# Kernel optimization log

Hardware: AMD Instinct MI355X
Metric: run time of the kernel (lower is better)

## Reference

```python
import jax, jax.numpy as jnp
import numpy as np

NPOINT = 2048  # S after transition-down (init npoint)
NSAMPLE = 16   # K neighbors (init nsample)
EPS = 1e-5     # BatchNorm eps


def _conv1d(w, b, x):  # w [O,I], x [B,I,N] -> [B,O,N]
    y = jnp.einsum('oi,bin->bon', w, x)
    return y if b is None else y + b[None, :, None]


def _conv2d(w, b, x):  # w [O,I], x [B,I,S,K] -> [B,O,S,K]
    y = jnp.einsum('oi,bisk->bosk', w, x)
    return y if b is None else y + b[None, :, None, None]


def _gather(x, idx):  # x [B,C,N], idx [B,S] -> [B,C,S]
    return jax.vmap(lambda xb, ib: xb[:, ib])(x, idx)


def _group(x, idx):  # x [B,C,N], idx [B,S,K] -> [B,C,S,K]
    return jax.vmap(lambda xb, ib: xb[:, ib])(x, idx)


def _fps(xyz_bnc, S):  # farthest point sampling, start at index 0 (deterministic)
    B, N, _ = xyz_bnc.shape
    def body(carry, _):
        dist, far = carry
        centroid = jnp.take_along_axis(xyz_bnc, far[:, None, None], axis=1)  # [B,1,3]
        d = jnp.sum((xyz_bnc - centroid) ** 2, axis=-1)  # [B,N]
        dist = jnp.minimum(dist, d)
        nxt = jnp.argmax(dist, axis=-1).astype(jnp.int32)
        return (dist, nxt), far
    init = (jnp.full((B, N), 1e10, xyz_bnc.dtype), jnp.zeros((B,), jnp.int32))
    _, idxs = jax.lax.scan(body, init, None, length=S)
    return jnp.transpose(idxs)  # [B,S]


def _knn(k, query, pts):  # query [B,S,3], pts [B,N,3] -> idx [B,S,k]
    d2 = (jnp.sum(query ** 2, -1)[..., None] + jnp.sum(pts ** 2, -1)[:, None, :]
          - 2.0 * jnp.einsum('bsc,bnc->bsn', query, pts))
    _, idx = jax.lax.top_k(-d2, k)
    return idx


def _bn(x, gamma, beta):  # training-mode batchnorm over (B, spatial) per channel
    axes = (0,) + tuple(range(2, x.ndim))
    m = jnp.mean(x, axes, keepdims=True)
    v = jnp.var(x, axes, keepdims=True)
    shp = (1, -1) + (1,) * (x.ndim - 2)
    return gamma.reshape(shp) * (x - m) / jnp.sqrt(v + EPS) + beta.reshape(shp)


def _forward(xyz, points, td_w, td_b, td_gamma, td_beta,
             blk_before_w, blk_before_b, blk_qkv_w,
             blk_pos_w1, blk_pos_b1, blk_pos_w2, blk_pos_b2,
             blk_attn_w1, blk_attn_b1, blk_attn_w2, blk_attn_b2,
             blk_after_w, blk_after_b):
    S, K = NPOINT, NSAMPLE
    xyz_t = jnp.transpose(xyz, (0, 2, 1))  # [B,N,3]
    # ---- PointTransformerTransitionDown ----
    fps_idx = _fps(xyz_t, S)                       # [B,S]
    new_xyz = _gather(xyz, fps_idx)                # [B,3,S]
    new_xyz_t = jnp.transpose(new_xyz, (0, 2, 1))  # [B,S,3]
    gidx = _knn(K, new_xyz_t, xyz_t)               # [B,S,K]
    grouped_xyz = _group(xyz, gidx) - new_xyz[:, :, :, None]   # [B,3,S,K]
    grouped = jnp.concatenate([_group(points, gidx), grouped_xyz], axis=1)  # [B,D+3,S,K]
    h = jax.nn.relu(_bn(_conv2d(td_w, td_b, grouped), td_gamma, td_beta))
    pts = jnp.max(h, axis=-1)  # [B,out,S]
    # ---- PointTransformerResBlocks ----
    sgidx = _knn(K, new_xyz_t, new_xyz_t)          # self-KNN [B,S,K]
    gxyz = new_xyz[:, :, :, None] - _group(new_xyz, sgidx)  # [B,3,S,K]
    num_attn = blk_before_w.shape[0]
    for i in range(num_attn):
        rel = _conv2d(blk_pos_w2[i], blk_pos_b2[i],
                      jax.nn.relu(_conv2d(blk_pos_w1[i], blk_pos_b1[i], gxyz)))  # [B,mid,S,K]
        p = _conv1d(blk_before_w[i], blk_before_b[i], pts)   # [B,mid,S]
        qkv = _conv1d(blk_qkv_w[i], None, p)                 # [B,3*mid,S]
        q, k_, v = jnp.split(qkv, 3, axis=1)
        qk_rel = q[:, :, :, None] - _group(k_, sgidx)        # [B,mid,S,K]
        v = _group(v, sgidx) + rel
        sim = _conv2d(blk_attn_w2[i], blk_attn_b2[i],
                      jax.nn.relu(_conv2d(blk_attn_w1[i], blk_attn_b1[i], qk_rel + rel)))
        attn = jax.nn.softmax(sim, axis=-1)                  # softmax over neighbors
        agg = jnp.sum(attn * v, axis=-1)                     # [B,mid,S]
        pts = pts + _conv1d(blk_after_w[i], blk_after_b[i], agg)
    return new_xyz, pts


def setup_inputs() -> dict:
    key = jax.random.key(0)
    ks = jax.random.split(key, 20)
    B, N, Din, Dout, mid, A = 4, 8192, 64, 128, 32, 2
    r = lambda k, s, sc: sc * jax.random.normal(k, s, dtype=jnp.float32)
    return {
        'xyz': r(ks[0], (B, 3, N), 1.0),
        'points': r(ks[1], (B, Din, N), 1.0),
        'td_w': r(ks[2], (Dout, Din + 3), 0.1), 'td_b': r(ks[3], (Dout,), 0.02),
        'td_gamma': jnp.ones((Dout,), jnp.float32), 'td_beta': jnp.zeros((Dout,), jnp.float32),
        'blk_before_w': r(ks[4], (A, mid, Dout), 0.1), 'blk_before_b': r(ks[5], (A, mid), 0.02),
        'blk_qkv_w': r(ks[6], (A, 3 * mid, mid), 0.1),
        'blk_pos_w1': r(ks[7], (A, 64, 3), 0.1), 'blk_pos_b1': r(ks[8], (A, 64), 0.02),
        'blk_pos_w2': r(ks[9], (A, mid, 64), 0.1), 'blk_pos_b2': r(ks[10], (A, mid), 0.02),
        'blk_attn_w1': r(ks[11], (A, 4 * mid, mid), 0.1), 'blk_attn_b1': r(ks[12], (A, 4 * mid), 0.02),
        'blk_attn_w2': r(ks[13], (A, mid, 4 * mid), 0.1), 'blk_attn_b2': r(ks[14], (A, mid), 0.02),
        'blk_after_w': r(ks[15], (A, Dout, mid), 0.1), 'blk_after_b': r(ks[16], (A, Dout), 0.02),
    }


def reference(xyz, points, td_w, td_b, td_gamma, td_beta,
              blk_before_w, blk_before_b, blk_qkv_w,
              blk_pos_w1, blk_pos_b1, blk_pos_w2, blk_pos_b2,
              blk_attn_w1, blk_attn_b1, blk_attn_w2, blk_attn_b2,
              blk_after_w, blk_after_b):
    return _forward(xyz, points, td_w, td_b, td_gamma, td_beta,
                    blk_before_w, blk_before_b, blk_qkv_w,
                    blk_pos_w1, blk_pos_b1, blk_pos_w2, blk_pos_b2,
                    blk_attn_w1, blk_attn_b1, blk_attn_w2, blk_attn_b2,
                    blk_after_w, blk_after_b)
```

## Files before the change

### kernel.cpp

```cpp
#include <hip/hip_runtime.h>

#define BB 4
#define NN 8192
#define SS 2048
#define KK 16

typedef float v2f __attribute__((ext_vector_type(2)));

#define FTH 512
#define FPT (NN/FTH)
__global__ __launch_bounds__(FTH, 1) void fps_kernel(
    const float* __restrict__ xyz,
    float* __restrict__ out_newxyz,
    float* __restrict__ nxt)
{
  #pragma clang fp contract(off)
  const int b = blockIdx.x;
  const int tid = threadIdx.x;
  const int wave = tid >> 6;
  const int lane = tid & 63;
  const float* xb = xyz + b*3*NN;
  __shared__ float sx[NN], sy[NN], sz[NN];
  __shared__ __align__(16) unsigned long long skey[2][8];
  __shared__ int smi[SS];
  v2f px[FPT/2], py[FPT/2], pz[FPT/2], dist[FPT/2];
  #pragma unroll
  for (int j = 0; j < FPT; ++j) {
    int i = tid + j*FTH;
    float x = xb[i], y = xb[NN+i], z = xb[2*NN+i];
    asm volatile("" : "+v"(x), "+v"(y), "+v"(z));
    ((float*)px)[j] = x; ((float*)py)[j] = y; ((float*)pz)[j] = z;
    ((float*)dist)[j] = 1e10f;
  }
  #pragma unroll
  for (int j = 0; j < FPT; ++j) {
    int i = tid + j*FTH;
    sx[i] = ((float*)px)[j]; sy[i] = ((float*)py)[j]; sz[i] = ((float*)pz)[j];
  }
  if (tid == 0) smi[0] = 0;
  int ic[FPT];
  #pragma unroll
  for (int j = 0; j < FPT; ++j) ic[j] = tid + j*FTH;
  float cx = xb[0], cy = xb[NN], cz = xb[2*NN];
  __syncthreads();
  for (int it = 1; it < SS; ++it) {
    const int buf = it & 1;
    v2f cx2 = {cx, cx}, cy2 = {cy, cy}, cz2 = {cz, cz};
    v2f vmax = {-1.0f, -1.0f};
    #pragma unroll
    for (int j = 0; j < FPT/2; ++j) {
      v2f dx = px[j] - cx2, dy = py[j] - cy2, dz = pz[j] - cz2;
      v2f d = dx*dx + dy*dy;
      d = d + dz*dz;
      v2f nd = __builtin_elementwise_min(dist[j], d);
      dist[j] = nd;
      vmax = __builtin_elementwise_max(vmax, nd);
    }
    float mloc = fmaxf(vmax.x, vmax.y);
    int besti = 0x7FFFFFFF;
    #pragma unroll
    for (int j = FPT/2 - 1; j >= 0; --j) {
      if (dist[j].y == mloc) besti = ic[2*j+1];
      if (dist[j].x == mloc) besti = ic[2*j];
    }
    unsigned khi = __float_as_uint(mloc);
    unsigned klo = ~(unsigned)besti;
    #define FPS_RED(ctrl) { \
      unsigned nlo = (unsigned)__builtin_amdgcn_update_dpp(0, (int)klo, ctrl, 0xf, 0xf, true); \
      unsigned nhi = (unsigned)__builtin_amdgcn_update_dpp(0, (int)khi, ctrl, 0xf, 0xf, true); \
      unsigned long long nk = ((unsigned long long)nhi << 32) | nlo; \
      unsigned long long ck = ((unsigned long long)khi << 32) | klo; \
      if (nk > ck) { khi = nhi; klo = nlo; } }
    FPS_RED(0x111)
    FPS_RED(0x112)
    FPS_RED(0x114)
    FPS_RED(0x118)
    FPS_RED(0x142)
    FPS_RED(0x143)
    #undef FPS_RED
    if (lane == 63) skey[buf][wave] = ((unsigned long long)khi << 32) | klo;
    __syncthreads();
    const ulonglong2* kp = (const ulonglong2*)&skey[buf][0];
    ulonglong2 k01 = kp[0], k23 = kp[1], k45 = kp[2], k67 = kp[3];
    unsigned long long m0 = k01.x > k01.y ? k01.x : k01.y;
    unsigned long long m1 = k23.x > k23.y ? k23.x : k23.y;
    unsigned long long m2 = k45.x > k45.y ? k45.x : k45.y;
    unsigned long long m3 = k67.x > k67.y ? k67.x : k67.y;
    unsigned long long ma = m0 > m1 ? m0 : m1;
    unsigned long long mb = m2 > m3 ? m2 : m3;
    unsigned long long mk = ma > mb ? ma : mb;
    int mi = (int)(~(unsigned)mk);
    if (tid == 0) smi[it] = mi;
    cx = sx[mi]; cy = sy[mi]; cz = sz[mi];
  }
  __syncthreads();
  for (int it = tid; it < SS; it += FTH) {
    int mi = smi[it];
    float x = sx[mi], y = sy[mi], z = sz[mi];
    out_newxyz[(b*3+0)*SS + it] = x;
    out_newxyz[(b*3+1)*SS + it] = y;
    out_newxyz[(b*3+2)*SS + it] = z;
    nxt[(b*SS+it)*3+0] = x; nxt[(b*SS+it)*3+1] = y; nxt[(b*SS+it)*3+2] = z;
  }
}

__global__ __launch_bounds__(256) void transpose_pts(
    const float* __restrict__ p, float* __restrict__ o)
{
  __shared__ float tile[32][33];
  const int b = blockIdx.z;
  const int n0 = blockIdx.x*32, c0 = blockIdx.y*32;
  const int x = threadIdx.x, y = threadIdx.y;
  #pragma unroll
  for (int i = y; i < 32; i += 8)
    tile[i][x] = p[(b*64 + c0+i)*NN + n0+x];
  __syncthreads();
  #pragma unroll
  for (int i = y; i < 32; i += 8)
    o[(b*NN + n0+i)*64 + c0+x] = tile[x][i];
}

#define TILE 2048
#define KTH 512
__global__ __launch_bounds__(KTH) void knn_kernel(
    const float* __restrict__ query_t,
    const float* __restrict__ cand1,
    const float* __restrict__ cand2,
    int* __restrict__ out1,
    int* __restrict__ out2)
{
  #pragma clang fp contract(off)
  __shared__ float4 sc[TILE];
  __shared__ float  smd[8*64*17];
  __shared__ int    smj[8*64*17];
  const int blocksPerB = SS/64;
  const int half = blockIdx.x >> 7;
  const int blk = blockIdx.x & 127;
  const float* cand = half ? cand2 : cand1;
  const int Nc = half ? SS : NN;
  int* outidx = half ? out2 : out1;
  const int b = blk / blocksPerB;
  const int q0 = (blk % blocksPerB)*64;
  const int wave = threadIdx.x >> 6, lane = threadIdx.x & 63;
  const int s = q0 + lane;
  const float qx = query_t[(b*SS+s)*3+0];
  const float qy = query_t[(b*SS+s)*3+1];
  const float qz = query_t[(b*SS+s)*3+2];
  float sq = qx*qx + qy*qy; sq = sq + qz*qz;
  float d16[16]; int i16[16];
  #pragma unroll
  for (int j = 0; j < 16; ++j) { d16[j] = 1e30f; i16[j] = 0x7FFFFFFF; }
  const float* cb = cand + b*3*Nc;
  const int QL = TILE/8;
  for (int base = 0; base < Nc; base += TILE) {
    __syncthreads();
    for (int j = threadIdx.x; j < TILE; j += KTH) {
      float x = cb[base+j], y = cb[Nc+base+j], z = cb[2*Nc+base+j];
      float pp = x*x + y*y; pp = pp + z*z;
      sc[j] = make_float4(x, y, z, pp);
    }
    __syncthreads();
    const int lo = wave*QL, hi = lo + QL;
    for (int j = lo; j < hi; ++j) {
      float4 c = sc[j];
      float qp = qx*c.x + qy*c.y; qp = qp + qz*c.z;
      float d2 = (sq + c.w) - 2.0f*qp;
      if (d2 < d16[15]) {
        d16[15] = d2; i16[15] = base + j;
        #pragma unroll
        for (int t = 15; t > 0; --t) {
          if (d16[t] < d16[t-1]) {
            float td = d16[t]; d16[t] = d16[t-1]; d16[t-1] = td;
            int   ti = i16[t]; i16[t] = i16[t-1]; i16[t-1] = ti;
          }
        }
      }
    }
  }
  const int off = (wave*64 + lane)*17;
  #pragma unroll
  for (int j = 0; j < 16; ++j) { smd[off+j] = d16[j]; smj[off+j] = i16[j]; }
  __syncthreads();
  if (wave == 0) {
    int p[8] = {0,0,0,0,0,0,0,0};
    for (int o = 0; o < 16; ++o) {
      float bd = 3e38f; int bi = 0x7FFFFFFF, bw = 0;
      #pragma unroll
      for (int w = 0; w < 8; ++w) {
        float d = smd[(w*64+lane)*17 + p[w]];
        int   i = smj[(w*64+lane)*17 + p[w]];
        if (d < bd || (d == bd && i < bi)) { bd = d; bi = i; bw = w; }
      }
      p[bw]++;
      outidx[(b*SS+s)*KK + o] = bi;
    }
  }
}

__global__ __launch_bounds__(128) void td_kernel(
    const float* __restrict__ ptst,
    const float* __restrict__ xyz,
    const float* __restrict__ newxyz,
    const int* __restrict__ gidx,
    const float* __restrict__ td_w,
    const float* __restrict__ td_b,
    float* __restrict__ ymax,
    float* __restrict__ psum,
    float* __restrict__ psq)
{
  const int bs = blockIdx.x;
  const int b = bs >> 11, s = bs & (SS-1);
  const int t = threadIdx.x;
  __shared__ int gi[KK];
  __shared__ float g[67*17];
  if (t < KK) gi[t] = gidx[bs*KK + t];
  __syncthreads();
  #pragma unroll
  for (int base = 0; base < 1024; base += 128) {
    int idx = base + t;
    int i = idx & 63, k = idx >> 6;
    g[i*17 + k] = ptst[(b*NN + gi[k])*64 + i];
  }
  if (t < 48) {
    int c = t >> 4, k = t & 15;
    g[(64+c)*17 + k] = xyz[(b*3+c)*NN + gi[k]] - newxyz[(b*3+c)*SS + s];
  }
  __syncthreads();
  float acc[KK];
  #pragma unroll
  for (int k = 0; k < KK; ++k) acc[k] = 0.0f;
  const float* wrow = td_w + t*67;
  for (int i = 0; i < 67; ++i) {
    float w = wrow[i];
    #pragma unroll
    for (int k = 0; k < KK; ++k) acc[k] = fmaf(w, g[i*17 + k], acc[k]);
  }
  float bias = td_b[t];
  float mx = -1e30f, s1 = 0.f, s2 = 0.f;
  #pragma unroll
  for (int k = 0; k < KK; ++k) {
    float y = acc[k] + bias;
    mx = fmaxf(mx, y);
    s1 += y;
    s2 = fmaf(y, y, s2);
  }
  ymax[bs*128 + t] = mx;
  psum[bs*128 + t] = s1;
  psq [bs*128 + t] = s2;
}

__global__ __launch_bounds__(256) void bn_partial(
    const float* __restrict__ psum, const float* __restrict__ psq,
    float* __restrict__ part1, float* __restrict__ part2)
{
  const int blk = blockIdx.x, t = threadIdx.x;
  const int c = t & 127, half = t >> 7;
  const float* ps = psum + (blk*64 + half*32)*128;
  const float* pq = psq  + (blk*64 + half*32)*128;
  float s1 = 0.f, s2 = 0.f;
  for (int r = 0; r < 32; ++r) { s1 += ps[r*128 + c]; s2 += pq[r*128 + c]; }
  __shared__ float sh1[256], sh2[256];
  sh1[t] = s1; sh2[t] = s2;
  __syncthreads();
  if (t < 128) {
    part1[blk*128 + t] = sh1[t] + sh1[t+128];
    part2[blk*128 + t] = sh2[t] + sh2[t+128];
  }
}

__global__ __launch_bounds__(128) void bn_final(
    const float* __restrict__ part1, const float* __restrict__ part2,
    const float* __restrict__ gamma, const float* __restrict__ beta,
    float* __restrict__ scale, float* __restrict__ bias)
{
  const int o = threadIdx.x;
  float s1 = 0.f, s2 = 0.f;
  for (int j = 0; j < 128; ++j) { s1 += part1[j*128+o]; s2 += part2[j*128+o]; }
  const float n = (float)(BB*SS*KK);
  float mean = s1/n;
  float var  = s2/n - mean*mean;
  float sc = gamma[o] / sqrtf(var + 1e-5f);
  scale[o] = sc;
  bias[o]  = beta[o] - mean*sc;
}

__global__ __launch_bounds__(128) void r1_first(
    const float* __restrict__ ymax,
    const float* __restrict__ scale, const float* __restrict__ bias,
    const float* __restrict__ bw, const float* __restrict__ bb,
    const float* __restrict__ qw,
    float* __restrict__ pts,
    float* __restrict__ qkv)
{
  const int bs = blockIdx.x;
  const int t = threadIdx.x;
  __shared__ float pcol[128];
  __shared__ float p[32];
  float v = fmaxf(fmaf(ymax[bs*128 + t], scale[t], bias[t]), 0.0f);
  pts[bs*128 + t] = v;
  pcol[t] = v;
  __syncthreads();
  if (t < 32) {
    float acc = 0.f;
    const float* w = bw + t*128;
    for (int j = 0; j < 128; ++j) acc = fmaf(w[j], pcol[j], acc);
    p[t] = acc + bb[t];
  }
  __syncthreads();
  if (t < 96) {
    float acc = 0.f;
    const float* w = qw + t*32;
    #pragma unroll
    for (int j = 0; j < 32; ++j) acc = fmaf(w[j], p[j], acc);
    qkv[bs*96 + t] = acc;
  }
}

__global__ __launch_bounds__(128) void r1_kernel(
    const float* __restrict__ pts,
    const float* __restrict__ bw, const float* __restrict__ bb,
    const float* __restrict__ qw,
    float* __restrict__ qkv)
{
  const int bs = blockIdx.x;
  const int t = threadIdx.x;
  __shared__ float pcol[128];
  __shared__ float p[32];
  pcol[t] = pts[bs*128 + t];
  __syncthreads();
  if (t < 32) {
    float acc = 0.f;
    const float* w = bw + t*128;
    for (int j = 0; j < 128; ++j) acc = fmaf(w[j], pcol[j], acc);
    p[t] = acc + bb[t];
  }
  __syncthreads();
  if (t < 96) {
    float acc = 0.f;
    const float* w = qw + t*32;
    #pragma unroll
    for (int j = 0; j < 32; ++j) acc = fmaf(w[j], p[j], acc);
    qkv[bs*96 + t] = acc;
  }
}

__global__ __launch_bounds__(128) void r2_kernel(
    const float* __restrict__ qkv,
    const float* __restrict__ newxyz,
    const int* __restrict__ sgidx,
    const float* __restrict__ pw1, const float* __restrict__ pb1,
    const float* __restrict__ pw2, const float* __restrict__ pb2,
    const float* __restrict__ aw1, const float* __restrict__ ab1,
    const float* __restrict__ aw2, const float* __restrict__ ab2,
    const float* __restrict__ fw,  const float* __restrict__ fb,
    float* __restrict__ pts)
{
  const int bs = blockIdx.x;
  const int b = bs >> 11, s = bs & (SS-1);
  const int t = threadIdx.x;
  __shared__ int sgi[KK];
  __shared__ float qv[32];
  __shared__ float kn[32*17], vn[32*17];
  __shared__ float gx[3*KK];
  __shared__ float h1[64*KK];
  __shared__ float x2[32*KK];
  __shared__ float a1[128*17];
  __shared__ float simb[32*KK];
  __shared__ float agg[32];
  if (t < KK) sgi[t] = sgidx[bs*KK + t];
  __syncthreads();
  if (t < 32) qv[t] = qkv[bs*96 + t];
  for (int idx = t; idx < 32*KK; idx += 128) {
    int k = idx >> 5, c = idx & 31;
    int base = (b*SS + sgi[k])*96;
    kn[c*17+k] = qkv[base + 32 + c];
    vn[c*17+k] = qkv[base + 64 + c];
  }
  if (t < 3*KK) {
    int c = t >> 4, k = t & 15;
    gx[t] = newxyz[(b*3+c)*SS + s] - newxyz[(b*3+c)*SS + sgi[k]];
  }
  __syncthreads();
  for (int idx = t; idx < 64*KK; idx += 128) {
    int c = idx >> 4, k = idx & 15;
    float acc = 0.f;
    #pragma unroll
    for (int j = 0; j < 3; ++j) acc = fmaf(pw1[c*3+j], gx[j*KK+k], acc);
    h1[idx] = fmaxf(acc + pb1[c], 0.0f);
  }
  __syncthreads();
  for (int idx = t; idx < 32*KK; idx += 128) {
    int c = idx >> 4, k = idx & 15;
    float acc = 0.f;
    const float* w = pw2 + c*64;
    for (int j = 0; j < 64; ++j) acc = fmaf(w[j], h1[j*KK+k], acc);
    float r = acc + pb2[c];
    x2[idx] = (qv[c] - kn[c*17+k]) + r;
    vn[c*17+k] = vn[c*17+k] + r;
  }
  __syncthreads();
  {
    float acc[KK];
    #pragma unroll
    for (int k = 0; k < KK; ++k) acc[k] = 0.f;
    const float* w = aw1 + t*32;
    for (int j = 0; j < 32; ++j) {
      float wv = w[j];
      #pragma unroll
      for (int k = 0; k < KK; ++k) acc[k] = fmaf(wv, x2[j*KK+k], acc[k]);
    }
    float bv = ab1[t];
    #pragma unroll
    for (int k = 0; k < KK; ++k) a1[t*17+k] = fmaxf(acc[k] + bv, 0.0f);
  }
  __syncthreads();
  for (int idx = t; idx < 32*KK; idx += 128) {
    int c = idx >> 4, k = idx & 15;
    float acc = 0.f;
    const float* w = aw2 + c*128;
    for (int j = 0; j < 128; ++j) acc = fmaf(w[j], a1[j*17+k], acc);
    simb[idx] = acc + ab2[c];
  }
  __syncthreads();
  if (t < 32) {
    float m = -1e30f;
    #pragma unroll
    for (int k = 0; k < KK; ++k) m = fmaxf(m, simb[t*KK+k]);
    float sum = 0.f;
    float e[KK];
    #pragma unroll
    for (int k = 0; k < KK; ++k) { e[k] = __expf(simb[t*KK+k] - m); sum += e[k]; }
    float inv = 1.0f / sum;
    float a = 0.f;
    #pragma unroll
    for (int k = 0; k < KK; ++k) a = fmaf(e[k]*inv, vn[t*17+k], a);
    agg[t] = a;
  }
  __syncthreads();
  {
    float acc = 0.f;
    const float* w = fw + t*32;
    #pragma unroll
    for (int j = 0; j < 32; ++j) acc = fmaf(w[j], agg[j], acc);
    pts[bs*128 + t] += acc + fb[t];
  }
}

__global__ __launch_bounds__(256) void transpose_out(
    const float* __restrict__ pts, float* __restrict__ out)
{
  __shared__ float tile[32][33];
  const int b = blockIdx.z;
  const int s0 = blockIdx.x*32, c0 = blockIdx.y*32;
  const int x = threadIdx.x, y = threadIdx.y;
  #pragma unroll
  for (int i = y; i < 32; i += 8)
    tile[i][x] = pts[(b*SS + s0+i)*128 + c0+x];
  __syncthreads();
  #pragma unroll
  for (int i = y; i < 32; i += 8)
    out[(b*128 + c0+i)*SS + s0 + x] = tile[x][i];
}

extern "C" void kernel_launch(void* const* d_in, const int* in_sizes, int n_in,
                              void* d_out, int out_size, void* d_ws, size_t ws_size,
                              hipStream_t stream) {
  const float* xyz      = (const float*)d_in[0];
  const float* points   = (const float*)d_in[1];
  const float* td_w     = (const float*)d_in[2];
  const float* td_b     = (const float*)d_in[3];
  const float* td_gamma = (const float*)d_in[4];
  const float* td_beta  = (const float*)d_in[5];
  const float* bw  = (const float*)d_in[6];
  const float* bb  = (const float*)d_in[7];
  const float* qw  = (const float*)d_in[8];
  const float* pw1 = (const float*)d_in[9];
  const float* pb1 = (const float*)d_in[10];
  const float* pw2 = (const float*)d_in[11];
  const float* pb2 = (const float*)d_in[12];
  const float* aw1 = (const float*)d_in[13];
  const float* ab1 = (const float*)d_in[14];
  const float* aw2 = (const float*)d_in[15];
  const float* ab2 = (const float*)d_in[16];
  const float* fw  = (const float*)d_in[17];
  const float* fb  = (const float*)d_in[18];
  float* out = (float*)d_out;
  float* out_newxyz = out;
  float* out_pts    = out + BB*3*SS;

  char* w = (char*)d_ws;
  float* nxt    = (float*)w; w += BB*SS*3*sizeof(float);
  int*   gidx   = (int*)w;   w += BB*SS*KK*sizeof(int);
  int*   sgidx  = (int*)w;   w += BB*SS*KK*sizeof(int);
  float* ymax   = (float*)w; w += BB*128*SS*sizeof(float);
  float* psum   = (float*)w; w += 128*BB*SS*sizeof(float);
  float* psq    = (float*)w; w += 128*BB*SS*sizeof(float);
  float* part1  = (float*)w; w += 128*128*sizeof(float);
  float* part2  = (float*)w; w += 128*128*sizeof(float);
  float* bnscale= (float*)w; w += 256*sizeof(float);
  float* bnbias = (float*)w; w += 256*sizeof(float);
  float* pts    = (float*)w; w += BB*128*SS*sizeof(float);
  float* qkv    = (float*)w; w += BB*96*SS*sizeof(float);
  float* ptst   = (float*)w; w += BB*NN*64*sizeof(float);

  fps_kernel<<<BB, FTH, 0, stream>>>(xyz, out_newxyz, nxt);
  {
    dim3 tg(NN/32, 2, BB), tb(32, 8);
    transpose_pts<<<tg, tb, 0, stream>>>(points, ptst);
  }
  knn_kernel<<<2*BB*(SS/64), KTH, 0, stream>>>(nxt, xyz, out_newxyz, gidx, sgidx);
  td_kernel<<<BB*SS, 128, 0, stream>>>(ptst, xyz, out_newxyz, gidx, td_w, td_b, ymax, psum, psq);
  bn_partial<<<128, 256, 0, stream>>>(psum, psq, part1, part2);
  bn_final<<<1, 128, 0, stream>>>(part1, part2, td_gamma, td_beta, bnscale, bnbias);
  r1_first<<<BB*SS, 128, 0, stream>>>(ymax, bnscale, bnbias, bw, bb, qw, pts, qkv);
  r2_kernel<<<BB*SS, 128, 0, stream>>>(qkv, out_newxyz, sgidx,
      pw1, pb1, pw2, pb2, aw1, ab1, aw2, ab2, fw, fb, pts);
  r1_kernel<<<BB*SS, 128, 0, stream>>>(pts, bw + 32*128, bb + 32, qw + 96*32, qkv);
  r2_kernel<<<BB*SS, 128, 0, stream>>>(qkv, out_newxyz, sgidx,
      pw1 + 64*3, pb1 + 64, pw2 + 32*64, pb2 + 32,
      aw1 + 128*32, ab1 + 128, aw2 + 32*128, ab2 + 32,
      fw + 128*32, fb + 128, pts);
  dim3 tg(SS/32, 128/32, BB), tb(32, 8);
  transpose_out<<<tg, tb, 0, stream>>>(pts, out_pts);
}
```

Measured before the change: 2.643 ms.

## Halve FPS block to 256 threads, pack xyz as float4, tree-reduce argmax index

The farthest-point-sampling kernel now runs 256 threads per batch, so each thread holds 32 points in registers and the cross-wave reduction merges only 4 wave keys. The three shared-memory coordinate arrays are packed into one float4 array so the centroid is fetched with a single load. The per-thread argmax index is found with a min-tree over local slot numbers instead of a serial scan against an index array, and the first-occurrence tie-break is kept. Fewer waves mean cheaper barriers and less reduction work per iteration, at the cost of more serial distance updates per thread and more register pressure.

```diff
diff --git a/kernel.cpp b/kernel.cpp
--- a/kernel.cpp
+++ b/kernel.cpp
@@ -7,7 +7,7 @@
 
 typedef float v2f __attribute__((ext_vector_type(2)));
 
-#define FTH 512
+#define FTH 256
 #define FPT (NN/FTH)
 __global__ __launch_bounds__(FTH, 1) void fps_kernel(
     const float* __restrict__ xyz,
@@ -20,8 +20,8 @@
   const int wave = tid >> 6;
   const int lane = tid & 63;
   const float* xb = xyz + b*3*NN;
-  __shared__ float sx[NN], sy[NN], sz[NN];
-  __shared__ __align__(16) unsigned long long skey[2][8];
+  __shared__ __align__(16) float4 sxyz[NN];
+  __shared__ __align__(16) unsigned long long skey[2][4];
   __shared__ int smi[SS];
   v2f px[FPT/2], py[FPT/2], pz[FPT/2], dist[FPT/2];
   #pragma unroll
@@ -31,16 +31,9 @@
     asm volatile("" : "+v"(x), "+v"(y), "+v"(z));
     ((float*)px)[j] = x; ((float*)py)[j] = y; ((float*)pz)[j] = z;
     ((float*)dist)[j] = 1e10f;
-  }
-  #pragma unroll
-  for (int j = 0; j < FPT; ++j) {
-    int i = tid + j*FTH;
-    sx[i] = ((float*)px)[j]; sy[i] = ((float*)py)[j]; sz[i] = ((float*)pz)[j];
+    sxyz[i] = make_float4(x, y, z, 0.0f);
   }
   if (tid == 0) smi[0] = 0;
-  int ic[FPT];
-  #pragma unroll
-  for (int j = 0; j < FPT; ++j) ic[j] = tid + j*FTH;
   float cx = xb[0], cy = xb[NN], cz = xb[2*NN];
   __syncthreads();
   for (int it = 1; it < SS; ++it) {
@@ -57,12 +50,20 @@
       vmax = __builtin_elementwise_max(vmax, nd);
     }
     float mloc = fmaxf(vmax.x, vmax.y);
-    int besti = 0x7FFFFFFF;
-    #pragma unroll
-    for (int j = FPT/2 - 1; j >= 0; --j) {
-      if (dist[j].y == mloc) besti = ic[2*j+1];
-      if (dist[j].x == mloc) besti = ic[2*j];
-    }
+    int ce[FPT/2];
+    #pragma unroll
+    for (int j = 0; j < FPT/2; ++j) {
+      int c = 0x7FFFFFFF;
+      if (dist[j].y == mloc) c = 2*j + 1;
+      if (dist[j].x == mloc) c = 2*j;
+      ce[j] = c;
+    }
+    #pragma unroll
+    for (int st = FPT/4; st >= 1; st >>= 1) {
+      #pragma unroll
+      for (int j = 0; j < st; ++j) ce[j] = ce[j] < ce[j+st] ? ce[j] : ce[j+st];
+    }
+    int besti = tid + (ce[0] << 8);
     unsigned khi = __float_as_uint(mloc);
     unsigned klo = ~(unsigned)besti;
     #define FPS_RED(ctrl) { \
@@ -81,26 +82,23 @@
     if (lane == 63) skey[buf][wave] = ((unsigned long long)khi << 32) | klo;
     __syncthreads();
     const ulonglong2* kp = (const ulonglong2*)&skey[buf][0];
-    ulonglong2 k01 = kp[0], k23 = kp[1], k45 = kp[2], k67 = kp[3];
+    ulonglong2 k01 = kp[0], k23 = kp[1];
     unsigned long long m0 = k01.x > k01.y ? k01.x : k01.y;
     unsigned long long m1 = k23.x > k23.y ? k23.x : k23.y;
-    unsigned long long m2 = k45.x > k45.y ? k45.x : k45.y;
-    unsigned long long m3 = k67.x > k67.y ? k67.x : k67.y;
-    unsigned long long ma = m0 > m1 ? m0 : m1;
-    unsigned long long mb = m2 > m3 ? m2 : m3;
-    unsigned long long mk = ma > mb ? ma : mb;
+    unsigned long long mk = m0 > m1 ? m0 : m1;
     int mi = (int)(~(unsigned)mk);
+    float4 c = sxyz[mi];
     if (tid == 0) smi[it] = mi;
-    cx = sx[mi]; cy = sy[mi]; cz = sz[mi];
+    cx = c.x; cy = c.y; cz = c.z;
   }
   __syncthreads();
   for (int it = tid; it < SS; it += FTH) {
     int mi = smi[it];
-    float x = sx[mi], y = sy[mi], z = sz[mi];
-    out_newxyz[(b*3+0)*SS + it] = x;
-    out_newxyz[(b*3+1)*SS + it] = y;
-    out_newxyz[(b*3+2)*SS + it] = z;
-    nxt[(b*SS+it)*3+0] = x; nxt[(b*SS+it)*3+1] = y; nxt[(b*SS+it)*3+2] = z;
+    float4 c = sxyz[mi];
+    out_newxyz[(b*3+0)*SS + it] = c.x;
+    out_newxyz[(b*3+1)*SS + it] = c.y;
+    out_newxyz[(b*3+2)*SS + it] = c.z;
+    nxt[(b*SS+it)*3+0] = c.x; nxt[(b*SS+it)*3+1] = c.y; nxt[(b*SS+it)*3+2] = c.z;
   }
 }
 
```

Result: no change. 2.611 ms (-1.2%).

## Morton-sort FPS points into per-thread cells and skip distance updates via bounding boxes

Applied to the files above, without the earlier changes.

The farthest-point-sampling kernel now computes the cloud's bounding box, buckets points into an 8x8x8 Morton grid with a shared-memory histogram and scan, and stores them as float4 in sorted order. Each thread therefore owns 16 spatially close points and keeps their bounding box. Each iteration, a thread skips its distance update when the box's lower-bound distance to the new centroid cannot beat its current max distance. This is meant to cut the per-iteration distance work, at the cost of setup overhead and divergence within a wave. Ties between equal distances are now broken by sorted position rather than original index, and the atomic-based placement order is nondeterministic.

```diff
diff --git a/kernel.cpp b/kernel.cpp
--- a/kernel.cpp
+++ b/kernel.cpp
@@ -20,51 +20,136 @@
   const int wave = tid >> 6;
   const int lane = tid & 63;
   const float* xb = xyz + b*3*NN;
-  __shared__ float sx[NN], sy[NN], sz[NN];
+  __shared__ __align__(16) float4 sxyz[NN];
   __shared__ __align__(16) unsigned long long skey[2][8];
   __shared__ int smi[SS];
-  v2f px[FPT/2], py[FPT/2], pz[FPT/2], dist[FPT/2];
+  __shared__ float sred[8*6];
+
+  float tx[FPT], ty[FPT], tz[FPT];
   #pragma unroll
   for (int j = 0; j < FPT; ++j) {
     int i = tid + j*FTH;
-    float x = xb[i], y = xb[NN+i], z = xb[2*NN+i];
-    asm volatile("" : "+v"(x), "+v"(y), "+v"(z));
-    ((float*)px)[j] = x; ((float*)py)[j] = y; ((float*)pz)[j] = z;
-    ((float*)dist)[j] = 1e10f;
-  }
+    tx[j] = xb[i]; ty[j] = xb[NN+i]; tz[j] = xb[2*NN+i];
+  }
+  float mnx = tx[0], mxx = tx[0], mny = ty[0], mxy = ty[0], mnz = tz[0], mxz = tz[0];
+  #pragma unroll
+  for (int j = 1; j < FPT; ++j) {
+    mnx = fminf(mnx, tx[j]); mxx = fmaxf(mxx, tx[j]);
+    mny = fminf(mny, ty[j]); mxy = fmaxf(mxy, ty[j]);
+    mnz = fminf(mnz, tz[j]); mxz = fmaxf(mxz, tz[j]);
+  }
+  #define WRED(var, OP) { \
+    float s_; \
+    s_ = __int_as_float(__builtin_amdgcn_update_dpp(0, __float_as_int(var), 0x111, 0xf, 0xf, true)); var = OP(var, s_); \
+    s_ = __int_as_float(__builtin_amdgcn_update_dpp(0, __float_as_int(var), 0x112, 0xf, 0xf, true)); var = OP(var, s_); \
+    s_ = __int_as_float(__builtin_amdgcn_update_dpp(0, __float_as_int(var), 0x114, 0xf, 0xf, true)); var = OP(var, s_); \
+    s_ = __int_as_float(__builtin_amdgcn_update_dpp(0, __float_as_int(var), 0x118, 0xf, 0xf, true)); var = OP(var, s_); \
+    s_ = __int_as_float(__builtin_amdgcn_update_dpp(0, __float_as_int(var), 0x142, 0xf, 0xf, true)); var = OP(var, s_); \
+    s_ = __int_as_float(__builtin_amdgcn_update_dpp(0, __float_as_int(var), 0x143, 0xf, 0xf, true)); var = OP(var, s_); }
+  WRED(mnx, fminf) WRED(mxx, fmaxf) WRED(mny, fminf) WRED(mxy, fmaxf) WRED(mnz, fminf) WRED(mxz, fmaxf)
+  #undef WRED
+  if (lane == 63) {
+    sred[wave*6+0] = mnx; sred[wave*6+1] = mxx; sred[wave*6+2] = mny;
+    sred[wave*6+3] = mxy; sred[wave*6+4] = mnz; sred[wave*6+5] = mxz;
+  }
+  smi[tid] = 0;
+  __syncthreads();
+  #pragma unroll
+  for (int w = 0; w < 8; ++w) {
+    mnx = fminf(mnx, sred[w*6+0]); mxx = fmaxf(mxx, sred[w*6+1]);
+    mny = fminf(mny, sred[w*6+2]); mxy = fmaxf(mxy, sred[w*6+3]);
+    mnz = fminf(mnz, sred[w*6+4]); mxz = fmaxf(mxz, sred[w*6+5]);
+  }
+  const float scx = 8.0f / (mxx - mnx + 1e-12f);
+  const float scy = 8.0f / (mxy - mny + 1e-12f);
+  const float scz = 8.0f / (mxz - mnz + 1e-12f);
+  int cells[FPT];
   #pragma unroll
   for (int j = 0; j < FPT; ++j) {
-    int i = tid + j*FTH;
-    sx[i] = ((float*)px)[j]; sy[i] = ((float*)py)[j]; sz[i] = ((float*)pz)[j];
-  }
-  if (tid == 0) smi[0] = 0;
-  int ic[FPT];
-  #pragma unroll
-  for (int j = 0; j < FPT; ++j) ic[j] = tid + j*FTH;
+    int qx = min(7, (int)((tx[j] - mnx) * scx));
+    int qy = min(7, (int)((ty[j] - mny) * scy));
+    int qz = min(7, (int)((tz[j] - mnz) * scz));
+    int m = (qx&1) | ((qy&1)<<1) | ((qz&1)<<2)
+          | ((qx&2)<<2) | ((qy&2)<<3) | ((qz&2)<<4)
+          | ((qx&4)<<4) | ((qy&4)<<5) | ((qz&4)<<6);
+    cells[j] = m;
+    atomicAdd(&smi[m], 1);
+  }
+  __syncthreads();
+  for (int d = 1; d < 512; d <<= 1) {
+    int v = smi[tid];
+    int a = (tid >= d) ? smi[tid - d] : 0;
+    __syncthreads();
+    smi[tid] = v + a;
+    __syncthreads();
+  }
+  {
+    int excl = (tid == 0) ? 0 : smi[tid - 1];
+    smi[512 + tid] = excl;
+  }
+  __syncthreads();
+  #pragma unroll
+  for (int j = 0; j < FPT; ++j) {
+    int pos = atomicAdd(&smi[512 + cells[j]], 1);
+    sxyz[pos] = make_float4(tx[j], ty[j], tz[j], 0.0f);
+  }
+  __syncthreads();
+  v2f px[FPT/2], py[FPT/2], pz[FPT/2], dist[FPT/2];
+  float bx0, bx1, by0, by1, bz0, bz1;
+  {
+    float4 c0 = sxyz[tid*FPT];
+    bx0 = bx1 = c0.x; by0 = by1 = c0.y; bz0 = bz1 = c0.z;
+    #pragma unroll
+    for (int e = 0; e < FPT; ++e) {
+      float4 cc = sxyz[tid*FPT + e];
+      ((float*)px)[e] = cc.x; ((float*)py)[e] = cc.y; ((float*)pz)[e] = cc.z;
+      ((float*)dist)[e] = 1e10f;
+      bx0 = fminf(bx0, cc.x); bx1 = fmaxf(bx1, cc.x);
+      by0 = fminf(by0, cc.y); by1 = fmaxf(by1, cc.y);
+      bz0 = fminf(bz0, cc.z); bz1 = fmaxf(bz1, cc.z);
+    }
+  }
+  float dmax = 1e10f;
+  int   beste = 0;
   float cx = xb[0], cy = xb[NN], cz = xb[2*NN];
   __syncthreads();
   for (int it = 1; it < SS; ++it) {
     const int buf = it & 1;
-    v2f cx2 = {cx, cx}, cy2 = {cy, cy}, cz2 = {cz, cz};
-    v2f vmax = {-1.0f, -1.0f};
-    #pragma unroll
-    for (int j = 0; j < FPT/2; ++j) {
-      v2f dx = px[j] - cx2, dy = py[j] - cy2, dz = pz[j] - cz2;
-      v2f d = dx*dx + dy*dy;
-      d = d + dz*dz;
-      v2f nd = __builtin_elementwise_min(dist[j], d);
-      dist[j] = nd;
-      vmax = __builtin_elementwise_max(vmax, nd);
+    float gx = fmaxf(fmaxf(bx0 - cx, cx - bx1), 0.0f);
+    float gy = fmaxf(fmaxf(by0 - cy, cy - by1), 0.0f);
+    float gz = fmaxf(fmaxf(bz0 - cz, cz - bz1), 0.0f);
+    float lb = gx*gx + gy*gy; lb = lb + gz*gz;
+    if (lb * 0.99999f < dmax) {
+      v2f cx2 = {cx, cx}, cy2 = {cy, cy}, cz2 = {cz, cz};
+      v2f vmax = {-1.0f, -1.0f};
+      #pragma unroll
+      for (int j = 0; j < FPT/2; ++j) {
+        v2f dx = px[j] - cx2, dy = py[j] - cy2, dz = pz[j] - cz2;
+        v2f d = dx*dx + dy*dy;
+        d = d + dz*dz;
+        v2f nd = __builtin_elementwise_min(dist[j], d);
+        dist[j] = nd;
+        vmax = __builtin_elementwise_max(vmax, nd);
+      }
+      float mloc = fmaxf(vmax.x, vmax.y);
+      int ce[FPT/2];
+      #pragma unroll
+      for (int j = 0; j < FPT/2; ++j) {
+        int c = 0x7FFFFFFF;
+        if (dist[j].y == mloc) c = 2*j + 1;
+        if (dist[j].x == mloc) c = 2*j;
+        ce[j] = c;
+      }
+      #pragma unroll
+      for (int st = FPT/4; st >= 1; st >>= 1) {
+        #pragma unroll
+        for (int j = 0; j < st; ++j) ce[j] = ce[j] < ce[j+st] ? ce[j] : ce[j+st];
+      }
+      dmax = mloc;
+      beste = ce[0];
     }
-    float mloc = fmaxf(vmax.x, vmax.y);
-    int besti = 0x7FFFFFFF;
-    #pragma unroll
-    for (int j = FPT/2 - 1; j >= 0; --j) {
-      if (dist[j].y == mloc) besti = ic[2*j+1];
-      if (dist[j].x == mloc) besti = ic[2*j];
-    }
-    unsigned khi = __float_as_uint(mloc);
-    unsigned klo = ~(unsigned)besti;
+    unsigned khi = __float_as_uint(dmax);
+    unsigned klo = ~(unsigned)((tid << 4) + beste);
     #define FPS_RED(ctrl) { \
       unsigned nlo = (unsigned)__builtin_amdgcn_update_dpp(0, (int)klo, ctrl, 0xf, 0xf, true); \
       unsigned nhi = (unsigned)__builtin_amdgcn_update_dpp(0, (int)khi, ctrl, 0xf, 0xf, true); \
@@ -90,13 +175,15 @@
     unsigned long long mb = m2 > m3 ? m2 : m3;
     unsigned long long mk = ma > mb ? ma : mb;
     int mi = (int)(~(unsigned)mk);
+    float4 c = sxyz[mi];
     if (tid == 0) smi[it] = mi;
-    cx = sx[mi]; cy = sy[mi]; cz = sz[mi];
+    cx = c.x; cy = c.y; cz = c.z;
   }
   __syncthreads();
   for (int it = tid; it < SS; it += FTH) {
-    int mi = smi[it];
-    float x = sx[mi], y = sy[mi], z = sz[mi];
+    float x, y, z;
+    if (it == 0) { x = xb[0]; y = xb[NN]; z = xb[2*NN]; }
+    else { float4 c = sxyz[smi[it]]; x = c.x; y = c.y; z = c.z; }
     out_newxyz[(b*3+0)*SS + it] = x;
     out_newxyz[(b*3+1)*SS + it] = y;
     out_newxyz[(b*3+2)*SS + it] = z;
```

Measured after the change: 2.476 ms. 6.3% less time.
